# Kernel optimization log

Measured on AMD Instinct MI355X. Metric: run time of the kernel, lower is better.

Reference implementation:

```python
import jax, jax.numpy as jnp
import numpy as np

# static config (matches init_kwargs)
NH, NKV, E, K = 16, 4, 8, 2
CAP_FACTOR = 1.25
LN_EPS = 1e-5


def _layer_norm(x, w, b):
    mu = jnp.mean(x, axis=-1, keepdims=True)
    var = jnp.mean(jnp.square(x - mu), axis=-1, keepdims=True)
    return (x - mu) * jax.lax.rsqrt(var + LN_EPS) * w + b


def setup_inputs() -> dict:
    key = jax.random.key(0)
    ks = jax.random.split(key, 6)
    S, B, H, F = 2048, 1, 1024, 2048
    HD = H // NH
    qkv_out = NKV * ((NH // NKV) + 2) * HD  # 1536
    f32 = jnp.float32
    return {
        "hidden_states": jax.random.normal(ks[0], (S, B, H), f32),
        "ln1_weight": jnp.ones((H,), f32),
        "ln1_bias": jnp.zeros((H,), f32),
        "ln2_weight": jnp.ones((H,), f32),
        "ln2_bias": jnp.zeros((H,), f32),
        "qkv_weight": jax.random.normal(ks[1], (qkv_out, H), f32) * 0.02,
        "proj_weight": jax.random.normal(ks[2], (H, H), f32) * 0.02,
        "router_weight": jax.random.normal(ks[3], (H, E), f32) * 0.02,
        "moe_w1": jax.random.normal(ks[4], (E, H, F), f32) * 0.02,
        "moe_w2": jax.random.normal(ks[5], (F and E, F, H), f32)[:E] * 0.02 if False else jax.random.normal(ks[5], (E, F, H), f32) * 0.02,
    }


def reference(hidden_states, ln1_weight, ln1_bias, ln2_weight, ln2_bias,
              qkv_weight, proj_weight, router_weight, moe_w1, moe_w2):
    S, B, H = hidden_states.shape
    HD = H // NH
    q_per_kv = NH // NKV
    # ---- attention block (cp_size=1: all-to-alls are identity) ----
    ln1 = _layer_norm(hidden_states, ln1_weight, ln1_bias)
    qkv = jnp.einsum('sbh,oh->sbo', ln1, qkv_weight)
    qkv = qkv.reshape(S, B, NKV, (q_per_kv + 2) * HD)
    q = qkv[..., : q_per_kv * HD].reshape(S, B, NH, HD)
    k = qkv[..., q_per_kv * HD:(q_per_kv + 1) * HD]          # [S,B,NKV,HD]
    v = qkv[..., (q_per_kv + 1) * HD:]                        # [S,B,NKV,HD]
    qb = jnp.transpose(q, (1, 2, 0, 3)).reshape(B, NKV, q_per_kv, S, HD)
    kb = jnp.transpose(k, (1, 2, 0, 3))                       # [B,NKV,S,HD]
    vb = jnp.transpose(v, (1, 2, 0, 3))
    scale = 1.0 / np.sqrt(HD).astype(np.float32)
    scores = jnp.einsum('bgqsd,bgtd->bgqst', qb, kb) * scale  # [B,NKV,qpk,S,S]
    causal = jnp.tril(jnp.ones((S, S), bool))
    scores = jnp.where(causal, scores, jnp.finfo(scores.dtype).min)
    attn = jax.nn.softmax(scores, axis=-1)
    ao = jnp.einsum('bgqst,bgtd->bgqsd', attn, vb)
    ao = ao.reshape(B, NH, S, HD)
    ao = jnp.transpose(ao, (2, 0, 1, 3)).reshape(S, B, H)
    proj = jnp.einsum('sbh,oh->sbo', ao, proj_weight)
    h1 = hidden_states + proj
    # ---- MoE block (ep_size=1: uniform all-to-all is identity) ----
    ln2 = _layer_norm(h1, ln2_weight, ln2_bias)
    x = ln2.reshape(-1, H)                                    # [N,H]
    N = x.shape[0]
    logits = x @ router_weight                                # linear(x, router_weight.t())
    probs = jax.nn.softmax(logits, axis=-1)
    top_p, top_i = jax.lax.top_k(probs, K)
    top_p = top_p / jnp.sum(top_p, axis=-1, keepdims=True)
    exp_idx = top_i.reshape(-1)                               # [N*K]
    exp_p = top_p.reshape(-1)
    # stable sort by expert id, capacity-padded dispatch
    order = jnp.argsort(exp_idx, stable=True)
    sorted_exp = exp_idx[order]
    counts = jnp.bincount(exp_idx, length=E)
    offsets = jnp.concatenate([jnp.zeros((1,), counts.dtype), jnp.cumsum(counts)[:-1]])
    within = jnp.arange(N * K) - offsets[sorted_exp]
    cap = int(np.ceil(N * K / E * CAP_FACTOR))
    T = E * cap
    valid = within < cap
    dst = jnp.where(valid, sorted_exp * cap + within, T)      # T = out-of-bounds -> dropped
    padded_tokens = jnp.zeros((T, H), x.dtype).at[dst].set(x[order // K], mode='drop')
    padded_probs = jnp.zeros((T,), exp_p.dtype).at[dst].set(exp_p[order], mode='drop')
    padded_tid = jnp.zeros((T,), jnp.int32).at[dst].set((order // K).astype(jnp.int32), mode='drop')
    # grouped expert GEMMs: [E,cap,H] x [E,H,F] -> gelu -> [E,cap,H]
    xt = padded_tokens.reshape(E, cap, H)
    fc1 = jax.nn.gelu(jnp.einsum('ech,ehf->ecf', xt, moe_w1))
    fc2 = jnp.einsum('ecf,efh->ech', fc1, moe_w2).reshape(T, H)
    weighted = fc2 * padded_probs[:, None]                    # pad slots have prob 0
    moe_out = jnp.zeros((N, H), hidden_states.dtype).at[padded_tid].add(weighted)
    return h1 + moe_out.reshape(S, B, H)
```

## Files before the change

### kernel.cpp

```cpp
#include <hip/hip_runtime.h>
#include <hip/hip_bf16.h>
#include <stdint.h>

#define S_LEN 2048
#define HDIM  1024
#define NHEAD 16
#define NKVH  4
#define HEADD 64
#define QKV_O 1536
#define NEXP  8
#define TOPK  2
#define CAP   640
#define TCAP  (NEXP*CAP)
#define FDIM  2048
#define LOG2E 1.44269504088896f
#define NCHUNK 40

typedef __bf16 bf16x8 __attribute__((ext_vector_type(8)));
typedef float  f32x4  __attribute__((ext_vector_type(4)));
typedef unsigned int u32;
typedef u32 u32x4 __attribute__((ext_vector_type(4)));
typedef u32 u32x2 __attribute__((ext_vector_type(2)));
typedef unsigned short u16;
typedef u16 u16x8 __attribute__((ext_vector_type(8)));

__device__ __forceinline__ void gload16(const __bf16* g, __bf16* l) {
    __builtin_amdgcn_global_load_lds(
        (const __attribute__((address_space(1))) u32*)g,
        (__attribute__((address_space(3))) u32*)l, 16, 0, 0);
}

__device__ __constant__ const signed char c_strip[NCHUNK] =
    {0,1,2,3, 4,4, 5,5, 6,6, 7,7, 8,8,8, 9,9,9, 10,10,10, 11,11,11,
     12,12,12,12, 13,13,13,13, 14,14,14,14, 15,15,15,15};
__device__ __constant__ const signed char c_chunk[NCHUNK] =
    {0,0,0,0, 0,1, 0,1, 0,1, 0,1, 0,1,2, 0,1,2, 0,1,2, 0,1,2,
     0,1,2,3, 0,1,2,3, 0,1,2,3, 0,1,2,3};
__device__ __constant__ const signed char c_cbase[16] = {0,1,2,3,4,6,8,10,12,15,18,21,24,28,32,36};
__device__ __constant__ const signed char c_nch[16]   = {1,1,1,1,2,2,2,2,3,3,3,3,4,4,4,4};

__global__ __launch_bounds__(256)
void prep_kernel(const float* __restrict__ hidden, const float* __restrict__ ln1w,
                 const float* __restrict__ ln1bb, const float* __restrict__ qkvW,
                 const float* __restrict__ projW, __bf16* __restrict__ ln1o,
                 __bf16* __restrict__ projWb, __bf16* __restrict__ qkvWb) {
    const int b = blockIdx.x, tid = threadIdx.x;
    if (b < S_LEN) {
        __shared__ float red[256];
        const float* x = hidden + (size_t)b * HDIM;
        float xr[4];
        #pragma unroll
        for (int j = 0; j < 4; ++j) xr[j] = x[tid + 256*j];
        float s = xr[0] + xr[1] + xr[2] + xr[3];
        red[tid] = s; __syncthreads();
        for (int st = 128; st > 0; st >>= 1) { if (tid < st) red[tid] += red[tid+st]; __syncthreads(); }
        float mu = red[0] / HDIM; __syncthreads();
        float v = 0.f;
        #pragma unroll
        for (int j = 0; j < 4; ++j) { float d = xr[j]-mu; v += d*d; }
        red[tid] = v; __syncthreads();
        for (int st = 128; st > 0; st >>= 1) { if (tid < st) red[tid] += red[tid+st]; __syncthreads(); }
        float rstd = rsqrtf(red[0]/HDIM + 1e-5f);
        #pragma unroll
        for (int j = 0; j < 4; ++j) {
            int i = tid + 256*j;
            ln1o[(size_t)b*HDIM + i] = (__bf16)((xr[j]-mu)*rstd*ln1w[i] + ln1bb[i]);
        }
        return;
    }
    const float* src; __bf16* dst; int i;
    if (b < S_LEN + 768) { src = qkvW; dst = qkvWb; i = (b - S_LEN)*256 + tid; }
    else                 { src = projW; dst = projWb; i = (b - S_LEN - 768)*256 + tid; }
    const float4* s = (const float4*)src + (size_t)i*2;
    float4 a = s[0], b4 = s[1];
    __bf16 tmp[8] = {(__bf16)a.x,(__bf16)a.y,(__bf16)a.z,(__bf16)a.w,
                     (__bf16)b4.x,(__bf16)b4.y,(__bf16)b4.z,(__bf16)b4.w};
    *(u32x4*)(dst + (size_t)i*8) = *(u32x4*)tmp;
}

__global__ __launch_bounds__(256)
void transp2_kernel(const float* __restrict__ w1, const float* __restrict__ w2,
                    __bf16* __restrict__ w1t, __bf16* __restrict__ w2t) {
    __shared__ float t[64][65];
    const int b = blockIdx.x;
    const float* src; __bf16* dst; int K, N, n0, k0;
    if (b < 4096) {
        int e = b >> 9, rem = b & 511;
        K = HDIM; N = FDIM; n0 = (rem & 31) * 64; k0 = (rem >> 5) * 64;
        src = w1 + (size_t)e*K*N; dst = w1t + (size_t)e*K*N;
    } else {
        int bb = b - 4096; int e = bb >> 9, rem = bb & 511;
        K = FDIM; N = HDIM; n0 = (rem & 15) * 64; k0 = (rem >> 4) * 64;
        src = w2 + (size_t)e*K*N; dst = w2t + (size_t)e*K*N;
    }
    const int tid = threadIdx.x;
    const int r = tid >> 4, c4 = (tid & 15) * 4;
    #pragma unroll
    for (int i = 0; i < 4; ++i) {
        float4 v = *(const float4*)(src + (size_t)(k0 + r + 16*i)*N + n0 + c4);
        t[r+16*i][c4+0] = v.x; t[r+16*i][c4+1] = v.y;
        t[r+16*i][c4+2] = v.z; t[r+16*i][c4+3] = v.w;
    }
    __syncthreads();
    const int rn = tid >> 3, kc = (tid & 7) * 8;
    #pragma unroll
    for (int i = 0; i < 2; ++i) {
        int n = rn + 32*i;
        __bf16 tmp[8];
        #pragma unroll
        for (int j = 0; j < 8; ++j) tmp[j] = (__bf16)t[kc+j][n];
        *(u32x4*)(dst + (size_t)(n0+n)*K + k0 + kc) = *(u32x4*)tmp;
    }
}

template<int EPI>
__global__ __launch_bounds__(256)
void gemm_bf16_kernel(const __bf16* __restrict__ A, const __bf16* __restrict__ Bt,
                      const float* __restrict__ R, void* __restrict__ Cout,
                      int N, int K, long sA, long sB, long sC) {
    __shared__ __bf16 As[128*64];
    __shared__ __bf16 Bs[128*64];
    const int e = blockIdx.z;
    A  += (size_t)e * sA;
    Bt += (size_t)e * sB;
    const int m0 = blockIdx.y*128, n0 = blockIdx.x*128;
    const int tid = threadIdx.x;
    const int lane = tid & 63, w = tid >> 6;
    const int lr = lane & 15, lg = lane >> 4;
    const int wr = w >> 1, wc = w & 1;
    const int srow8 = lane >> 3, sg = lane & 7;
    f32x4 acc[4][4] = {};
    for (int k0 = 0; k0 < K; k0 += 64) {
        __syncthreads();
        #pragma unroll
        for (int i = 0; i < 4; ++i) {
            int row = 32*w + 8*i + srow8;
            int src_g = sg ^ (row & 7);
            gload16(A  + (size_t)(m0+row)*K + k0 + src_g*8,
                    (__bf16*)((char*)As + (32*w + 8*i)*128));
            gload16(Bt + (size_t)(n0+row)*K + k0 + src_g*8,
                    (__bf16*)((char*)Bs + (32*w + 8*i)*128));
        }
        __syncthreads();
        #pragma unroll
        for (int ks = 0; ks < 2; ++ks) {
            bf16x8 af[4], bfr[4];
            #pragma unroll
            for (int mi = 0; mi < 4; ++mi) {
                int row = wr*64 + mi*16 + lr;
                af[mi] = *(const bf16x8*)((const char*)As + ((row*128 + (lg+4*ks)*16) ^ ((row&7)<<4)));
            }
            #pragma unroll
            for (int ni = 0; ni < 4; ++ni) {
                int row = wc*64 + ni*16 + lr;
                bfr[ni] = *(const bf16x8*)((const char*)Bs + ((row*128 + (lg+4*ks)*16) ^ ((row&7)<<4)));
            }
            #pragma unroll
            for (int mi = 0; mi < 4; ++mi)
                #pragma unroll
                for (int ni = 0; ni < 4; ++ni)
                    acc[mi][ni] = __builtin_amdgcn_mfma_f32_16x16x32_bf16(af[mi], bfr[ni], acc[mi][ni], 0,0,0);
        }
    }
    #pragma unroll
    for (int mi = 0; mi < 4; ++mi) {
        #pragma unroll
        for (int ni = 0; ni < 4; ++ni) {
            #pragma unroll
            for (int r = 0; r < 4; ++r) {
                int row = m0 + wr*64 + mi*16 + lg*4 + r;
                int col = n0 + wc*64 + ni*16 + lr;
                float v = acc[mi][ni][r];
                if (EPI == 1) v += R[(size_t)row*N + col];
                if (EPI == 2) {
                    float t = 0.7978845608028654f * (v + 0.044715f*v*v*v);
                    v = 0.5f * v * (1.f + tanhf(t));
                }
                if (EPI == 2 || EPI == 3)
                    ((__bf16*)Cout)[(size_t)e*sC + (size_t)row*N + col] = (__bf16)v;
                else
                    ((float*)Cout)[(size_t)e*sC + (size_t)row*N + col] = v;
            }
        }
    }
}

__global__ __launch_bounds__(512)
void attn_part_kernel(const __bf16* __restrict__ qkv, float* __restrict__ partO,
                      float* __restrict__ partML) {
    const int cx = blockIdx.x;
    const int h  = blockIdx.y;
    const int hg = h >> 2, qi = h & 3;
    const int qb = c_strip[cx];
    const int t0 = 4 * c_chunk[cx];
    const int t1 = min(qb + 1, t0 + 4);
    const int q0 = qb * 128;
    const int tid  = threadIdx.x;
    const int w    = tid >> 6;
    const int lane = tid & 63;
    const int lr   = lane & 15;
    const int lg   = lane >> 4;

    __shared__ __attribute__((aligned(16))) __bf16 Kls[128*64];
    __shared__ __attribute__((aligned(16))) __bf16 Vls[64*128];
    __shared__ __attribute__((aligned(16))) __bf16 Pls[8][16*128];

    const int krow = tid >> 2, kc = (tid & 3) * 2;
    const int va = tid & 63,  dg  = tid >> 6;
    u32x4 kreg[2]; u16x8 vreg[2];

    const __bf16* kbase = qkv + hg*384 + 256;
    const __bf16* vbase = qkv + hg*384 + 320;

#define ISSUE(T) do { \
        const __bf16* kp = kbase + (size_t)((T)*128 + krow)*QKV_O + kc*8; \
        kreg[0] = *(const u32x4*)(kp); \
        kreg[1] = *(const u32x4*)(kp + 8); \
        const __bf16* vp = vbase + (size_t)((T)*128 + 2*va)*QKV_O + dg*8; \
        vreg[0] = *(const u16x8*)(vp); \
        vreg[1] = *(const u16x8*)(vp + QKV_O); \
    } while(0)

#define COMMIT() do { \
        char* Kb = (char*)Kls; \
        *(u32x4*)(Kb + ((krow*128 + (kc+0)*16) ^ ((krow&7)<<4))) = kreg[0]; \
        *(u32x4*)(Kb + ((krow*128 + (kc+1)*16) ^ ((krow&7)<<4))) = kreg[1]; \
        char* Vb = (char*)Vls; \
        _Pragma("unroll") \
        for (int j = 0; j < 8; ++j) { \
            int d = dg*8 + j; \
            u32 u = ((u32)vreg[1][j] << 16) | vreg[0][j]; \
            *(u32*)(Vb + ((d*256 + va*4) ^ ((d&7)<<4))) = u; \
        } \
    } while(0)

    const int qrow = q0 + w*16 + lr;
    const __bf16* qp = qkv + (size_t)qrow*QKV_O + hg*384 + qi*64;
    bf16x8 qfrag[2];
    #pragma unroll
    for (int ks = 0; ks < 2; ++ks) {
        bf16x8 qr = *(const bf16x8*)(qp + ks*32 + lg*8);
        #pragma unroll
        for (int j = 0; j < 8; ++j) qfrag[ks][j] = (__bf16)((float)qr[j] * 0.125f);
    }
    bf16x8 ones;
    #pragma unroll
    for (int j = 0; j < 8; ++j) ones[j] = (__bf16)1.0f;

    f32x4 oacc[4] = {};
    f32x4 lcol = {};
    float mrow[4] = {-INFINITY,-INFINITY,-INFINITY,-INFINITY};

    ISSUE(t0);
    for (int t = t0; t < t1; ++t) {
        __syncthreads();
        COMMIT();
        if (t+1 < t1) ISSUE(t+1);
        __syncthreads();

        f32x4 sacc[8] = {};
        const char* Kb = (const char*)Kls;
        #pragma unroll
        for (int f = 0; f < 8; ++f) {
            int row = lr + 16*f;
            int swz = (row & 7) << 4;
            #pragma unroll
            for (int ks = 0; ks < 2; ++ks) {
                bf16x8 kf = *(const bf16x8*)(Kb + ((row*128 + (lg*8+32*ks)*2) ^ swz));
                sacc[f] = __builtin_amdgcn_mfma_f32_16x16x32_bf16(qfrag[ks], kf, sacc[f], 0,0,0);
            }
        }
        if (t == qb) {
            #pragma unroll
            for (int f = 0; f < 8; ++f)
                #pragma unroll
                for (int r = 0; r < 4; ++r)
                    if (lr + 16*f > 16*w + 4*lg + r) sacc[f][r] = -INFINITY;
        }
        float tm[4];
        #pragma unroll
        for (int r = 0; r < 4; ++r) {
            float a = fmaxf(fmaxf(sacc[0][r], sacc[1][r]), fmaxf(sacc[2][r], sacc[3][r]));
            float b2 = fmaxf(fmaxf(sacc[4][r], sacc[5][r]), fmaxf(sacc[6][r], sacc[7][r]));
            tm[r] = fmaxf(a, b2);
        }
        #pragma unroll
        for (int msk = 1; msk < 16; msk <<= 1)
            #pragma unroll
            for (int r = 0; r < 4; ++r) tm[r] = fmaxf(tm[r], __shfl_xor(tm[r], msk, 64));
        float corr[4];
        #pragma unroll
        for (int r = 0; r < 4; ++r) {
            float mn = fmaxf(mrow[r], tm[r]);
            corr[r] = exp2f((mrow[r]-mn)*LOG2E);
            mrow[r] = mn;
        }
        #pragma unroll
        for (int f = 0; f < 8; ++f)
            #pragma unroll
            for (int r = 0; r < 4; ++r)
                sacc[f][r] = exp2f((sacc[f][r]-mrow[r])*LOG2E);
        #pragma unroll
        for (int ct = 0; ct < 4; ++ct)
            #pragma unroll
            for (int r = 0; r < 4; ++r) oacc[ct][r] *= corr[r];
        #pragma unroll
        for (int r = 0; r < 4; ++r) lcol[r] *= corr[r];
        char* Pw = (char*)&Pls[w][0];
        #pragma unroll
        for (int f = 0; f < 8; ++f)
            #pragma unroll
            for (int r = 0; r < 4; ++r) {
                int row = 4*lg + r, col = lr + 16*f;
                *(__bf16*)(Pw + ((row*256 + col*2) ^ ((row&7)<<4))) = (__bf16)sacc[f][r];
            }
        const char* Vb = (const char*)Vls;
        bf16x8 pa[4];
        #pragma unroll
        for (int ks = 0; ks < 4; ++ks)
            pa[ks] = *(const bf16x8*)(Pw + ((lr*256 + (lg*8+32*ks)*2) ^ ((lr&7)<<4)));
        #pragma unroll
        for (int ks = 0; ks < 4; ++ks)
            lcol = __builtin_amdgcn_mfma_f32_16x16x32_bf16(pa[ks], ones, lcol, 0,0,0);
        #pragma unroll
        for (int ct = 0; ct < 4; ++ct) {
            int row = lr + 16*ct;
            int swz = (row & 7) << 4;
            #pragma unroll
            for (int ks = 0; ks < 4; ++ks) {
                bf16x8 vf = *(const bf16x8*)(Vb + ((row*256 + (lg*8+32*ks)*2) ^ swz));
                oacc[ct] = __builtin_amdgcn_mfma_f32_16x16x32_bf16(pa[ks], vf, oacc[ct], 0,0,0);
            }
        }
    }
    const int p = h*NCHUNK + cx;
    float* po = partO + (size_t)p * (128*64);
    #pragma unroll
    for (int ct = 0; ct < 4; ++ct)
        #pragma unroll
        for (int r = 0; r < 4; ++r)
            po[(16*w + 4*lg + r)*64 + 16*ct + lr] = oacc[ct][r];
    if (lr == 0) {
        float* pm = partML + (size_t)p * 256;
        #pragma unroll
        for (int r = 0; r < 4; ++r) {
            pm[(16*w + 4*lg + r)*2    ] = mrow[r];
            pm[(16*w + 4*lg + r)*2 + 1] = lcol[r];
        }
    }
#undef ISSUE
#undef COMMIT
}

__global__ __launch_bounds__(256)
void attn_combine_kernel(const float* __restrict__ partO, const float* __restrict__ partML,
                         __bf16* __restrict__ ao) {
    const int rb = blockIdx.x, h = blockIdx.y;
    const int row0 = rb*8;
    const int qb = row0 >> 7;
    const int nc = c_nch[qb], cb = c_cbase[qb];
    const int tid = threadIdx.x;
    const int rl = tid >> 5, d2 = (tid & 31) * 2;
    const int grow = row0 + rl;
    const int srow = grow & 127;
    const int pbase = h*NCHUNK + cb;
    float mv[4], lv[4];
    float M = -INFINITY;
    for (int c = 0; c < nc; ++c) {
        const float* pm = partML + (size_t)(pbase+c)*256 + srow*2;
        mv[c] = pm[0]; lv[c] = pm[1];
        M = fmaxf(M, mv[c]);
    }
    float L = 0.f, a0 = 0.f, a1 = 0.f;
    for (int c = 0; c < nc; ++c) {
        float wc = exp2f((mv[c]-M)*LOG2E);
        L += wc * lv[c];
        const float* po = partO + (size_t)(pbase+c)*(128*64) + srow*64 + d2;
        a0 += wc * po[0];
        a1 += wc * po[1];
    }
    float inv = 1.f / L;
    __bf16 o2[2] = {(__bf16)(a0*inv), (__bf16)(a1*inv)};
    *(u32*)(ao + (size_t)grow*HDIM + h*64 + d2) = *(u32*)o2;
}

__global__ __launch_bounds__(256)
void ln2_router_kernel(const float* __restrict__ h1, const float* __restrict__ w,
                       const float* __restrict__ b, const float* __restrict__ rw,
                       __bf16* __restrict__ x2b, int* __restrict__ expi,
                       float* __restrict__ expp) {
    const int t = blockIdx.x, tid = threadIdx.x;
    __shared__ float red[256];
    __shared__ float red8[256][8];
    const float* x = h1 + (size_t)t*HDIM;
    float xr[4];
    #pragma unroll
    for (int j = 0; j < 4; ++j) xr[j] = x[tid + 256*j];
    float s = xr[0] + xr[1] + xr[2] + xr[3];
    red[tid] = s; __syncthreads();
    for (int st = 128; st > 0; st >>= 1) { if (tid < st) red[tid] += red[tid+st]; __syncthreads(); }
    float mu = red[0] / HDIM; __syncthreads();
    float v = 0.f;
    #pragma unroll
    for (int j = 0; j < 4; ++j) { float d = xr[j]-mu; v += d*d; }
    red[tid] = v; __syncthreads();
    for (int st = 128; st > 0; st >>= 1) { if (tid < st) red[tid] += red[tid+st]; __syncthreads(); }
    float rstd = rsqrtf(red[0]/HDIM + 1e-5f);
    float part[8] = {};
    #pragma unroll
    for (int j = 0; j < 4; ++j) {
        int i = tid + 256*j;
        float o = (xr[j]-mu)*rstd*w[i] + b[i];
        x2b[(size_t)t*HDIM + i] = (__bf16)o;
        const float* wp = rw + (size_t)i*NEXP;
        #pragma unroll
        for (int e2 = 0; e2 < 8; ++e2) part[e2] += o * wp[e2];
    }
    #pragma unroll
    for (int e2 = 0; e2 < 8; ++e2) red8[tid][e2] = part[e2];
    __syncthreads();
    for (int st = 128; st > 0; st >>= 1) {
        if (tid < st)
            #pragma unroll
            for (int e2 = 0; e2 < 8; ++e2) red8[tid][e2] += red8[tid+st][e2];
        __syncthreads();
    }
    if (tid == 0) {
        float lg[8];
        #pragma unroll
        for (int e2 = 0; e2 < 8; ++e2) lg[e2] = red8[0][e2];
        int i0 = 0;
        for (int e2 = 1; e2 < 8; ++e2) if (lg[e2] > lg[i0]) i0 = e2;
        int i1 = -1;
        for (int e2 = 0; e2 < 8; ++e2) { if (e2 == i0) continue; if (i1 < 0 || lg[e2] > lg[i1]) i1 = e2; }
        float p1 = __expf(lg[i1] - lg[i0]);
        float inv = 1.f / (1.f + p1);
        expi[t*2]   = i0; expi[t*2+1] = i1;
        expp[t*2]   = inv; expp[t*2+1] = p1 * inv;
    }
}

__global__ __launch_bounds__(256)
void dst_fast_kernel(const int* __restrict__ expi, int* __restrict__ dst) {
    __shared__ int hist[256][9];
    const int tid = threadIdx.x;
    int ev[16];
    #pragma unroll
    for (int i = 0; i < 16; i += 4)
        *(int4*)(ev+i) = *(const int4*)(expi + tid*16 + i);
    int cnt[8] = {};
    #pragma unroll
    for (int i = 0; i < 16; ++i)
        #pragma unroll
        for (int e = 0; e < 8; ++e) cnt[e] += (ev[i] == e);
    #pragma unroll
    for (int e = 0; e < 8; ++e) hist[tid][e] = cnt[e];
    __syncthreads();
    const int w = tid >> 6, lane = tid & 63;
    #pragma unroll
    for (int rep = 0; rep < 2; ++rep) {
        int e = w + rep*4;
        int h0 = hist[4*lane+0][e], h1 = hist[4*lane+1][e],
            h2 = hist[4*lane+2][e], h3 = hist[4*lane+3][e];
        int s = h0+h1+h2+h3, inc = s;
        #pragma unroll
        for (int off = 1; off < 64; off <<= 1) {
            int v = __shfl_up(inc, off, 64);
            if (lane >= off) inc += v;
        }
        int excl = inc - s;
        hist[4*lane+0][e] = excl;
        hist[4*lane+1][e] = excl + h0;
        hist[4*lane+2][e] = excl + h0 + h1;
        hist[4*lane+3][e] = excl + h0 + h1 + h2;
    }
    __syncthreads();
    int run[8];
    #pragma unroll
    for (int e = 0; e < 8; ++e) run[e] = hist[tid][e];
    int out[16];
    #pragma unroll
    for (int i = 0; i < 16; ++i) {
        int e = ev[i], within = 0;
        #pragma unroll
        for (int e2 = 0; e2 < 8; ++e2)
            if (e == e2) { within = run[e2]; run[e2]++; }
        out[i] = (within < CAP) ? (e*CAP + within) : -1;
    }
    #pragma unroll
    for (int i = 0; i < 16; i += 4)
        *(int4*)(dst + tid*16 + i) = *(const int4*)(out+i);
}

__global__ void scatter_kernel(const __bf16* __restrict__ x2b, const int* __restrict__ dst,
                               __bf16* __restrict__ xt) {
    int s = blockIdx.x;
    int d = dst[s];
    if (d < 0) return;
    int t = s >> 1;
    int i = threadIdx.x;
    u32x2 v = *(const u32x2*)(x2b + (size_t)t*HDIM + i*4);
    *(u32x2*)(xt + (size_t)d*HDIM + i*4) = v;
}

__global__ void combine_kernel(const float* __restrict__ h1, const float* __restrict__ fc2,
                               const int* __restrict__ dst, const float* __restrict__ expp,
                               float* __restrict__ out) {
    int t = blockIdx.x;
    int d0 = dst[t*2], d1 = dst[t*2+1];
    float p0 = expp[t*2], p1 = expp[t*2+1];
    int i = threadIdx.x * 4;
    float4 v = *(const float4*)(h1 + (size_t)t*HDIM + i);
    if (d0 >= 0) {
        float4 f = *(const float4*)(fc2 + (size_t)d0*HDIM + i);
        v.x += p0*f.x; v.y += p0*f.y; v.z += p0*f.z; v.w += p0*f.w;
    }
    if (d1 >= 0) {
        float4 f = *(const float4*)(fc2 + (size_t)d1*HDIM + i);
        v.x += p1*f.x; v.y += p1*f.y; v.z += p1*f.z; v.w += p1*f.w;
    }
    *(float4*)(out + (size_t)t*HDIM + i) = v;
}

extern "C" void kernel_launch(void* const* d_in, const int* in_sizes, int n_in,
                              void* d_out, int out_size, void* d_ws, size_t ws_size,
                              hipStream_t stream) {
    const float* hidden = (const float*)d_in[0];
    const float* ln1w   = (const float*)d_in[1];
    const float* ln1b_  = (const float*)d_in[2];
    const float* ln2w   = (const float*)d_in[3];
    const float* ln2b_  = (const float*)d_in[4];
    const float* qkvW   = (const float*)d_in[5];
    const float* projW  = (const float*)d_in[6];
    const float* routW  = (const float*)d_in[7];
    const float* w1     = (const float*)d_in[8];
    const float* w2     = (const float*)d_in[9];
    float* out = (float*)d_out;

    char* base = (char*)d_ws;
    __bf16* w1t    = (__bf16*)(base);
    __bf16* w2t    = (__bf16*)(base + 33554432);
    __bf16* ln1b   = (__bf16*)(base + 0);
    __bf16* qkvWb  = (__bf16*)(base + 4194304);
    __bf16* qkvb   = (__bf16*)(base + 7340032);
    __bf16* aob    = (__bf16*)(base + 13631488);
    __bf16* projWb = (__bf16*)(base + 17825792);
    char* B0 = base + 67108864;
    float*  h1   = (float*)(B0);
    __bf16* xtb  = (__bf16*)(B0 + 8388608);
    __bf16* fc1b = (__bf16*)(B0 + 18874368);
    float*  fc2  = (float*)(B0 + 39845888);
    __bf16* x2b  = (__bf16*)fc2;
    int*    expi = (int*)(B0 + 60817408);
    int*    dsts = (int*)(B0 + 60833792);
    float*  expp = (float*)(B0 + 60850176);
    float*  partML = (float*)xtb;
    float*  partO  = (float*)fc1b;

    prep_kernel<<<S_LEN + 768 + 512, 256, 0, stream>>>(
        hidden, ln1w, ln1b_, qkvW, projW, ln1b, projWb, qkvWb);
    gemm_bf16_kernel<3><<<dim3(QKV_O/128, S_LEN/128, 1), 256, 0, stream>>>(
        ln1b, qkvWb, nullptr, qkvb, QKV_O, HDIM, 0, 0, 0);
    attn_part_kernel<<<dim3(NCHUNK, NHEAD), 512, 0, stream>>>(qkvb, partO, partML);
    attn_combine_kernel<<<dim3(S_LEN/8, NHEAD), 256, 0, stream>>>(partO, partML, aob);
    gemm_bf16_kernel<1><<<dim3(HDIM/128, S_LEN/128, 1), 256, 0, stream>>>(
        aob, projWb, hidden, h1, HDIM, HDIM, 0, 0, 0);
    ln2_router_kernel<<<S_LEN, 256, 0, stream>>>(h1, ln2w, ln2b_, routW, x2b, expi, expp);
    dst_fast_kernel<<<1, 256, 0, stream>>>(expi, dsts);
    scatter_kernel<<<S_LEN*TOPK, 256, 0, stream>>>(x2b, dsts, xtb);
    transp2_kernel<<<8192, 256, 0, stream>>>(w1, w2, w1t, w2t);
    gemm_bf16_kernel<2><<<dim3(FDIM/128, CAP/128, NEXP), 256, 0, stream>>>(
        xtb, w1t, nullptr, fc1b, FDIM, HDIM,
        (long)CAP*HDIM, (long)FDIM*HDIM, (long)CAP*FDIM);
    gemm_bf16_kernel<0><<<dim3(HDIM/128, CAP/128, NEXP), 256, 0, stream>>>(
        fc1b, w2t, nullptr, fc2, HDIM, FDIM,
        (long)CAP*FDIM, (long)FDIM*HDIM, (long)CAP*HDIM);
    combine_kernel<<<S_LEN, 256, 0, stream>>>(h1, fc2, dsts, expp, out);
}
```

Baseline: 250.2 us.

## Fuse expert weight fp32-to-bf16 transpose into grouped GEMM B-tile loads

Removes the separate transpose/convert pass over both MoE weight tensors. The expert GEMMs now read the fp32 weights directly in their original [K,N] layout, convert pairs to bf16 in registers and write them transposed into the swizzled shared-memory B tile. This saves a full read of the fp32 weights and a write plus re-read of the bf16 copies. In exchange, B-tile loads become synchronous, strided fp32 global loads instead of async direct-to-LDS loads. Each weight tile is also re-read by every M-block, which relies on cache reuse.

```diff
diff --git a/kernel.cpp b/kernel.cpp
--- a/kernel.cpp
+++ b/kernel.cpp
@@ -24,6 +24,10 @@
 typedef unsigned short u16;
 typedef u16 u16x8 __attribute__((ext_vector_type(8)));
 
+__device__ __forceinline__ u16 bfbits(float x) {
+    return __builtin_bit_cast(u16, (__bf16)x);
+}
+
 __device__ __forceinline__ void gload16(const __bf16* g, __bf16* l) {
     __builtin_amdgcn_global_load_lds(
         (const __attribute__((address_space(1))) u32*)g,
@@ -78,68 +82,57 @@
     *(u32x4*)(dst + (size_t)i*8) = *(u32x4*)tmp;
 }
 
+template<int EPI, int BSRC>
 __global__ __launch_bounds__(256)
-void transp2_kernel(const float* __restrict__ w1, const float* __restrict__ w2,
-                    __bf16* __restrict__ w1t, __bf16* __restrict__ w2t) {
-    __shared__ float t[64][65];
-    const int b = blockIdx.x;
-    const float* src; __bf16* dst; int K, N, n0, k0;
-    if (b < 4096) {
-        int e = b >> 9, rem = b & 511;
-        K = HDIM; N = FDIM; n0 = (rem & 31) * 64; k0 = (rem >> 5) * 64;
-        src = w1 + (size_t)e*K*N; dst = w1t + (size_t)e*K*N;
-    } else {
-        int bb = b - 4096; int e = bb >> 9, rem = bb & 511;
-        K = FDIM; N = HDIM; n0 = (rem & 15) * 64; k0 = (rem >> 4) * 64;
-        src = w2 + (size_t)e*K*N; dst = w2t + (size_t)e*K*N;
-    }
-    const int tid = threadIdx.x;
-    const int r = tid >> 4, c4 = (tid & 15) * 4;
-    #pragma unroll
-    for (int i = 0; i < 4; ++i) {
-        float4 v = *(const float4*)(src + (size_t)(k0 + r + 16*i)*N + n0 + c4);
-        t[r+16*i][c4+0] = v.x; t[r+16*i][c4+1] = v.y;
-        t[r+16*i][c4+2] = v.z; t[r+16*i][c4+3] = v.w;
-    }
-    __syncthreads();
-    const int rn = tid >> 3, kc = (tid & 7) * 8;
-    #pragma unroll
-    for (int i = 0; i < 2; ++i) {
-        int n = rn + 32*i;
-        __bf16 tmp[8];
-        #pragma unroll
-        for (int j = 0; j < 8; ++j) tmp[j] = (__bf16)t[kc+j][n];
-        *(u32x4*)(dst + (size_t)(n0+n)*K + k0 + kc) = *(u32x4*)tmp;
-    }
-}
-
-template<int EPI>
-__global__ __launch_bounds__(256)
-void gemm_bf16_kernel(const __bf16* __restrict__ A, const __bf16* __restrict__ Bt,
+void gemm_bf16_kernel(const __bf16* __restrict__ A, const void* __restrict__ Bsrc,
                       const float* __restrict__ R, void* __restrict__ Cout,
                       int N, int K, long sA, long sB, long sC) {
     __shared__ __bf16 As[128*64];
     __shared__ __bf16 Bs[128*64];
     const int e = blockIdx.z;
-    A  += (size_t)e * sA;
-    Bt += (size_t)e * sB;
+    A += (size_t)e * sA;
+    const __bf16* Bt = (const __bf16*)Bsrc + (BSRC == 0 ? (size_t)e * sB : 0);
+    const float*  Wf = (const float*)Bsrc + (BSRC == 1 ? (size_t)e * sB : 0);
     const int m0 = blockIdx.y*128, n0 = blockIdx.x*128;
     const int tid = threadIdx.x;
     const int lane = tid & 63, w = tid >> 6;
     const int lr = lane & 15, lg = lane >> 4;
     const int wr = w >> 1, wc = w & 1;
     const int srow8 = lane >> 3, sg = lane & 7;
+    const int b2 = tid & 7, kp = tid >> 3;
     f32x4 acc[4][4] = {};
     for (int k0 = 0; k0 < K; k0 += 64) {
         __syncthreads();
-        #pragma unroll
-        for (int i = 0; i < 4; ++i) {
-            int row = 32*w + 8*i + srow8;
-            int src_g = sg ^ (row & 7);
-            gload16(A  + (size_t)(m0+row)*K + k0 + src_g*8,
-                    (__bf16*)((char*)As + (32*w + 8*i)*128));
-            gload16(Bt + (size_t)(n0+row)*K + k0 + src_g*8,
-                    (__bf16*)((char*)Bs + (32*w + 8*i)*128));
+        if (BSRC == 0) {
+            #pragma unroll
+            for (int i = 0; i < 4; ++i) {
+                int row = 32*w + 8*i + srow8;
+                int src_g = sg ^ (row & 7);
+                gload16(A  + (size_t)(m0+row)*K + k0 + src_g*8,
+                        (__bf16*)((char*)As + (32*w + 8*i)*128));
+                gload16(Bt + (size_t)(n0+row)*K + k0 + src_g*8,
+                        (__bf16*)((char*)Bs + (32*w + 8*i)*128));
+            }
+        } else {
+            #pragma unroll
+            for (int i = 0; i < 4; ++i) {
+                int row = 32*w + 8*i + srow8;
+                int src_g = sg ^ (row & 7);
+                gload16(A + (size_t)(m0+row)*K + k0 + src_g*8,
+                        (__bf16*)((char*)As + (32*w + 8*i)*128));
+            }
+            const int k = 2*kp;
+            const float* w0 = Wf + (size_t)(k0+k)*N + n0 + b2*2;
+            #pragma unroll
+            for (int j = 0; j < 8; ++j) {
+                float2 r0 = *(const float2*)(w0 + 16*j);
+                float2 r1 = *(const float2*)(w0 + N + 16*j);
+                int n = b2*2 + 16*j;
+                u32 u0 = ((u32)bfbits(r1.x) << 16) | bfbits(r0.x);
+                u32 u1 = ((u32)bfbits(r1.y) << 16) | bfbits(r0.y);
+                *(u32*)((char*)Bs + ((n*128 + k*2) ^ ((n&7)<<4))) = u0;
+                *(u32*)((char*)Bs + (((n+1)*128 + k*2) ^ (((n+1)&7)<<4))) = u1;
+            }
         }
         __syncthreads();
         #pragma unroll
@@ -538,8 +531,6 @@
     float* out = (float*)d_out;
 
     char* base = (char*)d_ws;
-    __bf16* w1t    = (__bf16*)(base);
-    __bf16* w2t    = (__bf16*)(base + 33554432);
     __bf16* ln1b   = (__bf16*)(base + 0);
     __bf16* qkvWb  = (__bf16*)(base + 4194304);
     __bf16* qkvb   = (__bf16*)(base + 7340032);
@@ -559,21 +550,20 @@
 
     prep_kernel<<<S_LEN + 768 + 512, 256, 0, stream>>>(
         hidden, ln1w, ln1b_, qkvW, projW, ln1b, projWb, qkvWb);
-    gemm_bf16_kernel<3><<<dim3(QKV_O/128, S_LEN/128, 1), 256, 0, stream>>>(
+    gemm_bf16_kernel<3,0><<<dim3(QKV_O/128, S_LEN/128, 1), 256, 0, stream>>>(
         ln1b, qkvWb, nullptr, qkvb, QKV_O, HDIM, 0, 0, 0);
     attn_part_kernel<<<dim3(NCHUNK, NHEAD), 512, 0, stream>>>(qkvb, partO, partML);
     attn_combine_kernel<<<dim3(S_LEN/8, NHEAD), 256, 0, stream>>>(partO, partML, aob);
-    gemm_bf16_kernel<1><<<dim3(HDIM/128, S_LEN/128, 1), 256, 0, stream>>>(
+    gemm_bf16_kernel<1,0><<<dim3(HDIM/128, S_LEN/128, 1), 256, 0, stream>>>(
         aob, projWb, hidden, h1, HDIM, HDIM, 0, 0, 0);
     ln2_router_kernel<<<S_LEN, 256, 0, stream>>>(h1, ln2w, ln2b_, routW, x2b, expi, expp);
     dst_fast_kernel<<<1, 256, 0, stream>>>(expi, dsts);
     scatter_kernel<<<S_LEN*TOPK, 256, 0, stream>>>(x2b, dsts, xtb);
-    transp2_kernel<<<8192, 256, 0, stream>>>(w1, w2, w1t, w2t);
-    gemm_bf16_kernel<2><<<dim3(FDIM/128, CAP/128, NEXP), 256, 0, stream>>>(
-        xtb, w1t, nullptr, fc1b, FDIM, HDIM,
-        (long)CAP*HDIM, (long)FDIM*HDIM, (long)CAP*FDIM);
-    gemm_bf16_kernel<0><<<dim3(HDIM/128, CAP/128, NEXP), 256, 0, stream>>>(
-        fc1b, w2t, nullptr, fc2, HDIM, FDIM,
+    gemm_bf16_kernel<2,1><<<dim3(FDIM/128, CAP/128, NEXP), 256, 0, stream>>>(
+        xtb, w1, nullptr, fc1b, FDIM, HDIM,
+        (long)CAP*HDIM, (long)HDIM*FDIM, (long)CAP*FDIM);
+    gemm_bf16_kernel<0,1><<<dim3(HDIM/128, CAP/128, NEXP), 256, 0, stream>>>(
+        fc1b, w2, nullptr, fc2, HDIM, FDIM,
         (long)CAP*FDIM, (long)FDIM*HDIM, (long)CAP*HDIM);
     combine_kernel<<<S_LEN, 256, 0, stream>>>(h1, fc2, dsts, expp, out);
 }
```

Result: slower. 263.7 us (+5.4%).
